# Optimization experiments

Hardware: AMD Instinct MI355X
Metric: run time of the kernel (lower is better)

## Reference

```python
import jax, jax.numpy as jnp
import numpy as np

N, E, D, H = 50000, 1600000, 256, 256
EPS = 1e-5

def prelu(x, a):
    return jnp.where(x >= 0, x, a * x)

def batch_norm(x, gamma, beta):
    # training-mode BatchNorm1d: stats over the node (batch) dim
    mu = jnp.mean(x, axis=0)
    var = jnp.var(x, axis=0)
    return (x - mu) * jax.lax.rsqrt(var + EPS) * gamma + beta

def gcn_conv(x, edge_index, W, b):
    # PyG GCNConv: h = XW, add self-loops, symmetric norm, scatter-add, + bias
    h = x @ W
    n = x.shape[0]
    row = jnp.concatenate([edge_index[0], jnp.arange(n)])
    col = jnp.concatenate([edge_index[1], jnp.arange(n)])
    w = jnp.ones(row.shape[0], dtype=x.dtype)
    deg = jax.ops.segment_sum(w, col, num_segments=n)
    dinv = jnp.where(deg > 0, jax.lax.rsqrt(deg), 0.0)
    norm = dinv[row] * w * dinv[col]  # [E+N]
    msg = h[row] * norm[:, None]      # [E+N, H] gathered messages
    out = jax.ops.segment_sum(msg, col, num_segments=n)
    return out + b

def setup_inputs() -> dict:
    key = jax.random.key(0)
    ks = jax.random.split(key, 10)
    x = jax.random.normal(ks[0], (N, D), dtype=jnp.float32)
    edge_index = jax.random.randint(ks[1], (2, E), 0, N).astype(jnp.int64)
    s1 = 1.0 / np.sqrt(D)
    s2 = 1.0 / np.sqrt(H)
    return {
        "x": x,
        "edge_index": edge_index,
        "W1": jax.random.uniform(ks[2], (D, H), jnp.float32, -s1, s1),
        "b1": jnp.zeros((H,), jnp.float32),
        "W2": jax.random.uniform(ks[3], (H, H), jnp.float32, -s2, s2),
        "b2": jnp.zeros((H,), jnp.float32),
        "prelu_a": jnp.asarray(0.25, jnp.float32),
        "bn_gamma": jnp.ones((H,), jnp.float32),
        "bn_beta": jnp.zeros((H,), jnp.float32),
        "proj_W": jax.random.uniform(ks[4], (H, H), jnp.float32, -s2, s2),
        "proj_b": jnp.zeros((H,), jnp.float32),
        "pbn_gamma": jnp.ones((H,), jnp.float32),
        "pbn_beta": jnp.zeros((H,), jnp.float32),
        "prelu2_a": jnp.asarray(0.25, jnp.float32),
    }

def reference(x, edge_index, W1, b1, W2, b2, prelu_a, bn_gamma, bn_beta,
              proj_W, proj_b, pbn_gamma, pbn_beta, prelu2_a):
    # eval-mode dropout (identity); BN uses batch stats
    z = prelu(gcn_conv(x, edge_index, W1, b1), prelu_a)
    z = prelu(gcn_conv(z, edge_index, W2, b2), prelu_a)
    z = batch_norm(z, bn_gamma, bn_beta)
    p = prelu(batch_norm(z @ proj_W + proj_b, pbn_gamma, pbn_beta), prelu2_a)
    return (z, p)
```

## Files before the change

kernel.cpp:

```cpp
#include <hip/hip_runtime.h>
#include <hip/hip_bf16.h>


#define CAP 96
#define NPB 128
#define CHUNK 4096
#define SEGBIG 4608
#define MAXBKT 512

typedef __attribute__((ext_vector_type(8))) short short8;
typedef __attribute__((ext_vector_type(4))) float f32x4;

__device__ __forceinline__ float bf2f(unsigned short u) {
    union { unsigned int i; float f; } v; v.i = ((unsigned int)u) << 16; return v.f;
}
__device__ __forceinline__ unsigned short f2bf(float f) {
    __hip_bfloat16 h = __float2bfloat16(f);
    return *reinterpret_cast<unsigned short*>(&h);
}

__global__ __launch_bounds__(256) void k_zero(int* segcnt, int nbkt, float* stats, float* dinv, int N) {
    int i = blockIdx.x * 256 + threadIdx.x;
    if (i < nbkt) segcnt[i] = 0;
    if (i < 2048) stats[i] = 0.0f;
    if (i == 0) dinv[N] = 0.0f;
}

__global__ __launch_bounds__(256) void k_zrow(unsigned short* hs, int N) {
    ((ushort4*)hs)[(size_t)N * 64 + threadIdx.x % 64] = ushort4{0, 0, 0, 0};
}

__global__ __launch_bounds__(256) void k_binh(const int* __restrict__ row, const int* __restrict__ col,
                                              unsigned* __restrict__ bins, int* __restrict__ segcnt,
                                              int E, int nbkt) {
    __shared__ int hist[MAXBKT];
    __shared__ int base[MAXBKT];
    int e0 = blockIdx.x * CHUNK;
    int eend = e0 + CHUNK; if (eend > E) eend = E;
    for (int b = threadIdx.x; b < nbkt; b += 256) hist[b] = 0;
    __syncthreads();
    for (int e = e0 + threadIdx.x; e < eend; e += 256)
        atomicAdd(&hist[col[e] >> 7], 1);
    __syncthreads();
    for (int b = threadIdx.x; b < nbkt; b += 256) {
        int h = hist[b];
        base[b] = h ? atomicAdd(&segcnt[b], h) : 0;
        hist[b] = 0;
    }
    __syncthreads();
    for (int e = e0 + threadIdx.x; e < eend; e += 256) {
        int v = col[e], r = row[e];
        int b = v >> 7;
        int p = base[b] + atomicAdd(&hist[b], 1);
        if (p < SEGBIG) bins[(size_t)b * SEGBIG + p] = ((unsigned)r << 7) | (unsigned)(v & (NPB - 1));
    }
}

__global__ __launch_bounds__(256) void k_csr(const unsigned* __restrict__ bins, const int* __restrict__ segcnt,
                                             int* __restrict__ csr, int* __restrict__ fillp,
                                             float* __restrict__ dinv, int N) {
    __shared__ int cnt[NPB];
    int bkt = blockIdx.x;
    if (threadIdx.x < NPB) cnt[threadIdx.x] = 0;
    __syncthreads();
    int m = segcnt[bkt]; if (m > SEGBIG) m = SEGBIG;
    const unsigned* b = bins + (size_t)bkt * SEGBIG;
    for (int i = threadIdx.x; i < m; i += 256) {
        unsigned ent = b[i];
        int loc = (int)(ent & (NPB - 1));
        int r   = (int)(ent >> 7);
        int p = atomicAdd(&cnt[loc], 1);
        if (p < CAP) csr[(size_t)(bkt * NPB + loc) * CAP + p] = r;
    }
    __syncthreads();
    if (threadIdx.x < NPB) {
        int v = bkt * NPB + threadIdx.x;
        if (v < N) {
            int c = cnt[threadIdx.x];
            int real = c < CAP ? c : CAP;
            int pc = (real + 15) & ~15;
            if (pc > CAP) pc = CAP;
            int* lst = csr + (size_t)v * CAP;
            for (int p = real; p < pc; ++p) lst[p] = N;
            fillp[v] = pc;
            dinv[v] = rsqrtf(1.0f + (float)c);
        }
    }
}

__global__ __launch_bounds__(256) void k_castx(const float* __restrict__ x, unsigned short* __restrict__ xb, size_t n4) {
    size_t stride = (size_t)gridDim.x * blockDim.x;
    for (size_t i = (size_t)blockIdx.x * blockDim.x + threadIdx.x; i < n4; i += stride) {
        float4 v = ((const float4*)x)[i];
        ushort4 o; o.x = f2bf(v.x); o.y = f2bf(v.y); o.z = f2bf(v.z); o.w = f2bf(v.w);
        ((ushort4*)xb)[i] = o;
    }
}

__global__ __launch_bounds__(256) void k_wt(const float* __restrict__ W, unsigned short* __restrict__ Wt) {
    __shared__ float t[32][33];
    int bx = blockIdx.x * 32, by = blockIdx.y * 32;
    int x = threadIdx.x & 31, y = threadIdx.x >> 5;
#pragma unroll
    for (int i = 0; i < 32; i += 8)
        t[y + i][x] = W[(size_t)(by + y + i) * 256 + bx + x];
    __syncthreads();
#pragma unroll
    for (int i = 0; i < 32; i += 8)
        Wt[(size_t)(bx + y + i) * 256 + by + x] = f2bf(t[x][y + i]);
}

__global__ __launch_bounds__(256) void k_gemm_bf16(const unsigned short* __restrict__ A,
                                                   const unsigned short* __restrict__ Bt,
                                                   unsigned short* __restrict__ C,
                                                   const float* __restrict__ dinv,
                                                   int use_scale, int M) {
    __shared__ unsigned short buf[16384];
    unsigned short* As = buf;
    unsigned short* Bs = buf + 8192;
    int tid  = threadIdx.x;
    int lane = tid & 63, wid = tid >> 6;
    int wr = wid >> 1, wc = wid & 1;
    int row0 = blockIdx.x * 128;
    int col0 = blockIdx.y * 128;

    f32x4 acc[4][4];
#pragma unroll
    for (int m = 0; m < 4; ++m)
#pragma unroll
        for (int n = 0; n < 4; ++n) acc[m][n] = f32x4{0.f, 0.f, 0.f, 0.f};

    int srow = lane >> 3;
    int sk   = (lane & 7) * 8;

    for (int k0 = 0; k0 < 256; k0 += 64) {
#pragma unroll
        for (int i = 0; i < 4; ++i) {
            int u = i * 4 + wid;
            int arow = row0 + u * 8 + srow;
            if (arow >= M) arow = M - 1;
            const unsigned short* ga = A  + (size_t)arow * 256 + k0 + sk;
            const unsigned short* gb = Bt + (size_t)(col0 + u * 8 + srow) * 256 + k0 + sk;
            __builtin_amdgcn_global_load_lds((const __attribute__((address_space(1))) void*)ga,
                (__attribute__((address_space(3))) void*)(As + u * 512), 16, 0, 0);
            __builtin_amdgcn_global_load_lds((const __attribute__((address_space(1))) void*)gb,
                (__attribute__((address_space(3))) void*)(Bs + u * 512), 16, 0, 0);
        }
        __syncthreads();
#pragma unroll
        for (int kk = 0; kk < 64; kk += 32) {
            short8 a[4], b[4];
#pragma unroll
            for (int m = 0; m < 4; ++m)
                a[m] = *(const short8*)(As + (wr * 64 + m * 16 + (lane & 15)) * 64 + kk + (lane >> 4) * 8);
#pragma unroll
            for (int n = 0; n < 4; ++n)
                b[n] = *(const short8*)(Bs + (wc * 64 + n * 16 + (lane & 15)) * 64 + kk + (lane >> 4) * 8);
#pragma unroll
            for (int m = 0; m < 4; ++m)
#pragma unroll
                for (int n = 0; n < 4; ++n)
                    acc[m][n] = __builtin_amdgcn_mfma_f32_16x16x32_bf16(a[m], b[n], acc[m][n], 0, 0, 0);
        }
        __syncthreads();
    }

#pragma unroll
    for (int m = 0; m < 4; ++m)
#pragma unroll
        for (int r = 0; r < 4; ++r) {
            int lr = wr * 64 + m * 16 + (lane >> 4) * 4 + r;
#pragma unroll
            for (int n = 0; n < 4; ++n)
                buf[lr * 128 + wc * 64 + n * 16 + (lane & 15)] = f2bf(acc[m][n][r]);
        }
    __syncthreads();
#pragma unroll
    for (int j = 0; j < 8; ++j) {
        int c = j * 256 + tid;
        int r = c >> 4, cc = c & 15;
        int grow = row0 + r;
        if (grow < M) {
            short8 v = *(const short8*)(buf + r * 128 + cc * 8);
            if (use_scale) {
                float d = dinv[grow];
                short8 o;
#pragma unroll
                for (int t = 0; t < 8; ++t)
                    o[t] = (short)f2bf(bf2f((unsigned short)v[t]) * d);
                v = o;
            }
            *(short8*)(C + (size_t)grow * 256 + col0 + cc * 8) = v;
        }
    }
}

__global__ __launch_bounds__(256) void k_agg_bf(const unsigned short* __restrict__ hs,
                                                unsigned short* __restrict__ outb,
                                                const float* __restrict__ dinv, const int* __restrict__ csr,
                                                const int* __restrict__ fillp, const float* __restrict__ bias,
                                                const float* __restrict__ aptr, int N) {
    int wv = threadIdx.x >> 6, lane = threadIdx.x & 63;
    int v = blockIdx.x * 4 + wv;
    if (v >= N) return;
    const ushort4* h4 = (const ushort4*)hs;
    float dv = dinv[v];
    ushort4 hv = h4[(size_t)v * 64 + lane];
    float s0 = bf2f(hv.x), s1 = bf2f(hv.y), s2 = bf2f(hv.z), s3 = bf2f(hv.w);
    int n = fillp[v];
    const int* lst = csr + (size_t)v * CAP;
    for (int i = 0; i < n; i += 16) {
        int u[16];
        ushort4 a[16];
#pragma unroll
        for (int t = 0; t < 16; ++t) u[t] = lst[i + t];
#pragma unroll
        for (int t = 0; t < 16; ++t) a[t] = h4[(size_t)u[t] * 64 + lane];
#pragma unroll
        for (int t = 0; t < 16; ++t) {
            s0 += bf2f(a[t].x); s1 += bf2f(a[t].y);
            s2 += bf2f(a[t].z); s3 += bf2f(a[t].w);
        }
    }
    float al = *aptr;
    float4 bb = *(const float4*)(bias + lane * 4);
    float o0 = dv * s0 + bb.x, o1 = dv * s1 + bb.y, o2 = dv * s2 + bb.z, o3 = dv * s3 + bb.w;
    o0 = o0 >= 0.f ? o0 : al * o0;
    o1 = o1 >= 0.f ? o1 : al * o1;
    o2 = o2 >= 0.f ? o2 : al * o2;
    o3 = o3 >= 0.f ? o3 : al * o3;
    ushort4 o; o.x = f2bf(o0); o.y = f2bf(o1); o.z = f2bf(o2); o.w = f2bf(o3);
    ((ushort4*)outb)[(size_t)v * 64 + lane] = o;
}

__global__ __launch_bounds__(256) void k_bnstats_v(const unsigned short* __restrict__ X, float* __restrict__ sums, int N) {
    int w = threadIdx.x >> 6, lane = threadIdx.x & 63;
    int c4 = lane * 4;
    float4 s = {0.f, 0.f, 0.f, 0.f}, q = {0.f, 0.f, 0.f, 0.f};
    int rstride = gridDim.x * 4;
    for (int r = blockIdx.x * 4 + w; r < N; r += rstride) {
        ushort4 x4 = ((const ushort4*)X)[(size_t)r * 64 + lane];
        float a = bf2f(x4.x), b = bf2f(x4.y), c = bf2f(x4.z), d = bf2f(x4.w);
        s.x += a; s.y += b; s.z += c; s.w += d;
        q.x += a * a; q.y += b * b; q.z += c * c; q.w += d * d;
    }
    atomicAdd(&sums[c4 + 0], s.x); atomicAdd(&sums[c4 + 1], s.y);
    atomicAdd(&sums[c4 + 2], s.z); atomicAdd(&sums[c4 + 3], s.w);
    atomicAdd(&sums[256 + c4 + 0], q.x); atomicAdd(&sums[256 + c4 + 1], q.y);
    atomicAdd(&sums[256 + c4 + 2], q.z); atomicAdd(&sums[256 + c4 + 3], q.w);
}

__global__ __launch_bounds__(256) void k_bnfinal(float* stats, const float* __restrict__ gamma,
                                                 const float* __restrict__ beta, float invN) {
    int c = threadIdx.x;
    float mu = stats[c] * invN;
    float var = stats[256 + c] * invN - mu * mu;
    float rstd = rsqrtf(var + 1e-5f);
    float sc = rstd * gamma[c];
    stats[512 + c] = sc;
    stats[768 + c] = beta[c] - mu * sc;
}

__global__ __launch_bounds__(256) void k_bnapply_z(const unsigned short* __restrict__ in,
                                                   float* __restrict__ zout, unsigned short* __restrict__ zb,
                                                   const float* __restrict__ scale, const float* __restrict__ shift,
                                                   size_t n4) {
    size_t stride = (size_t)gridDim.x * blockDim.x;
    for (size_t i = (size_t)blockIdx.x * blockDim.x + threadIdx.x; i < n4; i += stride) {
        int c4 = (int)(i & 63) * 4;
        ushort4 x4 = ((const ushort4*)in)[i];
        float4 sc = *(const float4*)(scale + c4);
        float4 sh = *(const float4*)(shift + c4);
        float4 y;
        y.x = bf2f(x4.x) * sc.x + sh.x;
        y.y = bf2f(x4.y) * sc.y + sh.y;
        y.z = bf2f(x4.z) * sc.z + sh.z;
        y.w = bf2f(x4.w) * sc.w + sh.w;
        ((float4*)zout)[i] = y;
        ushort4 o; o.x = f2bf(y.x); o.y = f2bf(y.y); o.z = f2bf(y.z); o.w = f2bf(y.w);
        ((ushort4*)zb)[i] = o;
    }
}

__global__ __launch_bounds__(256) void k_bnapply_p(const unsigned short* __restrict__ in,
                                                   float* __restrict__ pout,
                                                   const float* __restrict__ scale, const float* __restrict__ shift,
                                                   const float* __restrict__ aptr, size_t n4) {
    size_t stride = (size_t)gridDim.x * blockDim.x;
    float a = *aptr;
    for (size_t i = (size_t)blockIdx.x * blockDim.x + threadIdx.x; i < n4; i += stride) {
        int c4 = (int)(i & 63) * 4;
        ushort4 x4 = ((const ushort4*)in)[i];
        float4 sc = *(const float4*)(scale + c4);
        float4 sh = *(const float4*)(shift + c4);
        float4 y;
        y.x = bf2f(x4.x) * sc.x + sh.x;
        y.y = bf2f(x4.y) * sc.y + sh.y;
        y.z = bf2f(x4.z) * sc.z + sh.z;
        y.w = bf2f(x4.w) * sc.w + sh.w;
        y.x = y.x >= 0.f ? y.x : a * y.x;
        y.y = y.y >= 0.f ? y.y : a * y.y;
        y.z = y.z >= 0.f ? y.z : a * y.z;
        y.w = y.w >= 0.f ? y.w : a * y.w;
        ((float4*)pout)[i] = y;
    }
}

extern "C" void kernel_launch(void* const* d_in, const int* in_sizes, int n_in,
                              void* d_out, int out_size, void* d_ws, size_t ws_size,
                              hipStream_t stream) {
    const float* x     = (const float*)d_in[0];
    const int*   ei    = (const int*)d_in[1];
    const float* W1    = (const float*)d_in[2];
    const float* b1    = (const float*)d_in[3];
    const float* W2    = (const float*)d_in[4];
    const float* b2    = (const float*)d_in[5];
    const float* aptr  = (const float*)d_in[6];
    const float* gamma = (const float*)d_in[7];
    const float* beta  = (const float*)d_in[8];
    const float* projW = (const float*)d_in[9];
    const float* pgamma = (const float*)d_in[11];
    const float* pbeta  = (const float*)d_in[12];
    const float* a2ptr  = (const float*)d_in[13];

    int N = in_sizes[0] / 256;
    int E = in_sizes[1] / 2;
    const int* row = ei;
    const int* col = ei + E;

    float* out  = (float*)d_out;
    float* zout = out;
    float* pout = out + (size_t)N * 256;

    int nbkt = (N + NPB - 1) / NPB;

    size_t rowsz = (size_t)(N + 1) * 256;
    unsigned short* B0 = (unsigned short*)d_ws;
    unsigned short* B1 = B0 + rowsz;
    unsigned short* B2 = B1 + rowsz;
    unsigned short* Wt = B2 + rowsz;
    float* dinv  = (float*)(Wt + 3 * 65536);
    int*   fillp = (int*)(dinv + N + 1);
    int*   csr   = fillp + N;
    float* stats = (float*)(csr + (size_t)N * CAP);
    int*   segcnt= (int*)(stats + 2048);
    unsigned* bins = (unsigned*)(segcnt + MAXBKT);

    int nb_binh = (E + CHUNK - 1) / CHUNK;
    dim3 ggrid((N + 127) / 128, 2);
    dim3 wgrid(8, 8);
    int  agrid = (N + 3) / 4;
    size_t n4 = (size_t)N * 64;

    k_zero <<<8, 256, 0, stream>>>(segcnt, nbkt, stats, dinv, N);
    k_zrow <<<1, 64, 0, stream>>>(B1, N);
    k_binh <<<nb_binh, 256, 0, stream>>>(row, col, bins, segcnt, E, nbkt);
    k_csr  <<<nbkt, 256, 0, stream>>>(bins, segcnt, csr, fillp, dinv, N);
    k_castx<<<2048, 256, 0, stream>>>(x, B0, n4);
    k_wt   <<<wgrid, 256, 0, stream>>>(W1,    Wt);
    k_wt   <<<wgrid, 256, 0, stream>>>(W2,    Wt + 65536);
    k_wt   <<<wgrid, 256, 0, stream>>>(projW, Wt + 131072);

    k_gemm_bf16<<<ggrid, 256, 0, stream>>>(B0, Wt, B1, dinv, 1, N);
    k_agg_bf   <<<agrid, 256, 0, stream>>>(B1, B2, dinv, csr, fillp, b1, aptr, N);
    k_zrow <<<1, 64, 0, stream>>>(B1, N);
    k_gemm_bf16<<<ggrid, 256, 0, stream>>>(B2, Wt + 65536, B1, dinv, 1, N);
    k_agg_bf   <<<agrid, 256, 0, stream>>>(B1, B0, dinv, csr, fillp, b2, aptr, N);
    k_bnstats_v<<<128, 256, 0, stream>>>(B0, stats, N);
    k_bnfinal  <<<1, 256, 0, stream>>>(stats, gamma, beta, 1.0f / (float)N);
    k_bnapply_z<<<2048, 256, 0, stream>>>(B0, zout, B2, stats + 512, stats + 768, n4);
    k_gemm_bf16<<<ggrid, 256, 0, stream>>>(B2, Wt + 131072, B1, dinv, 0, N);
    k_bnstats_v<<<128, 256, 0, stream>>>(B1, stats + 1024, N);
    k_bnfinal  <<<1, 256, 0, stream>>>(stats + 1024, pgamma, pbeta, 1.0f / (float)N);
    k_bnapply_p<<<2048, 256, 0, stream>>>(B1, pout, stats + 1536, stats + 1792, a2ptr, n4);
}
```

Baseline: 677.3 us.

## Fold first BatchNorm into projection weights and refine edge binning granularity

The BN scale is folded into the transposed projection weights, and the shift becomes a per-column bias vector computed by a small kernel and added in the GEMM epilogue. This lets the projection GEMM read the pre-BN aggregate directly, and removes the bf16 write of the normalized z. Edge binning now uses 64-node buckets with smaller chunks, and the per-bucket counters are padded to separate cache lines to reduce atomic contention. It also drops one zero-row launch and the dinv[N] initialization. The trade-offs are an extra serial 256-thread matvec kernel, and bf16 rounding now applied to the pre-BN values times folded weights, which changes numerics slightly.

```diff
diff --git a/kernel.cpp b/kernel.cpp
--- a/kernel.cpp
+++ b/kernel.cpp
@@ -3,10 +3,11 @@
 
 
 #define CAP 96
-#define NPB 128
-#define CHUNK 4096
-#define SEGBIG 4608
-#define MAXBKT 512
+#define NPB 64
+#define CHUNK 2048
+#define SEGBIG 2432
+#define MAXBKT 1024
+#define SEGSTR 16
 
 typedef __attribute__((ext_vector_type(8))) short short8;
 typedef __attribute__((ext_vector_type(4))) float f32x4;
@@ -19,15 +20,14 @@
     return *reinterpret_cast<unsigned short*>(&h);
 }
 
-__global__ __launch_bounds__(256) void k_zero(int* segcnt, int nbkt, float* stats, float* dinv, int N) {
+__global__ __launch_bounds__(256) void k_zero(int* segcnt, int nbkt, float* stats) {
     int i = blockIdx.x * 256 + threadIdx.x;
-    if (i < nbkt) segcnt[i] = 0;
+    if (i < nbkt * SEGSTR) segcnt[i] = 0;
     if (i < 2048) stats[i] = 0.0f;
-    if (i == 0) dinv[N] = 0.0f;
-}
-
-__global__ __launch_bounds__(256) void k_zrow(unsigned short* hs, int N) {
-    ((ushort4*)hs)[(size_t)N * 64 + threadIdx.x % 64] = ushort4{0, 0, 0, 0};
+}
+
+__global__ __launch_bounds__(64) void k_zrow(unsigned short* hs, int N) {
+    ((ushort4*)hs)[(size_t)N * 64 + threadIdx.x] = ushort4{0, 0, 0, 0};
 }
 
 __global__ __launch_bounds__(256) void k_binh(const int* __restrict__ row, const int* __restrict__ col,
@@ -40,19 +40,19 @@
     for (int b = threadIdx.x; b < nbkt; b += 256) hist[b] = 0;
     __syncthreads();
     for (int e = e0 + threadIdx.x; e < eend; e += 256)
-        atomicAdd(&hist[col[e] >> 7], 1);
+        atomicAdd(&hist[col[e] >> 6], 1);
     __syncthreads();
     for (int b = threadIdx.x; b < nbkt; b += 256) {
         int h = hist[b];
-        base[b] = h ? atomicAdd(&segcnt[b], h) : 0;
+        base[b] = h ? atomicAdd(&segcnt[b * SEGSTR], h) : 0;
         hist[b] = 0;
     }
     __syncthreads();
     for (int e = e0 + threadIdx.x; e < eend; e += 256) {
         int v = col[e], r = row[e];
-        int b = v >> 7;
+        int b = v >> 6;
         int p = base[b] + atomicAdd(&hist[b], 1);
-        if (p < SEGBIG) bins[(size_t)b * SEGBIG + p] = ((unsigned)r << 7) | (unsigned)(v & (NPB - 1));
+        if (p < SEGBIG) bins[(size_t)b * SEGBIG + p] = ((unsigned)r << 6) | (unsigned)(v & (NPB - 1));
     }
 }
 
@@ -63,12 +63,12 @@
     int bkt = blockIdx.x;
     if (threadIdx.x < NPB) cnt[threadIdx.x] = 0;
     __syncthreads();
-    int m = segcnt[bkt]; if (m > SEGBIG) m = SEGBIG;
+    int m = segcnt[bkt * SEGSTR]; if (m > SEGBIG) m = SEGBIG;
     const unsigned* b = bins + (size_t)bkt * SEGBIG;
     for (int i = threadIdx.x; i < m; i += 256) {
         unsigned ent = b[i];
         int loc = (int)(ent & (NPB - 1));
-        int r   = (int)(ent >> 7);
+        int r   = (int)(ent >> 6);
         int p = atomicAdd(&cnt[loc], 1);
         if (p < CAP) csr[(size_t)(bkt * NPB + loc) * CAP + p] = r;
     }
@@ -97,24 +97,36 @@
     }
 }
 
-__global__ __launch_bounds__(256) void k_wt(const float* __restrict__ W, unsigned short* __restrict__ Wt) {
+__global__ __launch_bounds__(256) void k_wt(const float* __restrict__ W, unsigned short* __restrict__ Wt,
+                                            const float* __restrict__ scp) {
     __shared__ float t[32][33];
     int bx = blockIdx.x * 32, by = blockIdx.y * 32;
     int x = threadIdx.x & 31, y = threadIdx.x >> 5;
 #pragma unroll
-    for (int i = 0; i < 32; i += 8)
-        t[y + i][x] = W[(size_t)(by + y + i) * 256 + bx + x];
+    for (int i = 0; i < 32; i += 8) {
+        float s = scp ? scp[by + y + i] : 1.0f;
+        t[y + i][x] = W[(size_t)(by + y + i) * 256 + bx + x] * s;
+    }
     __syncthreads();
 #pragma unroll
     for (int i = 0; i < 32; i += 8)
         Wt[(size_t)(bx + y + i) * 256 + by + x] = f2bf(t[x][y + i]);
+}
+
+__global__ __launch_bounds__(256) void k_tvec(const float* __restrict__ W, const float* __restrict__ sh,
+                                              float* __restrict__ tvec) {
+    int n = threadIdx.x;
+    float s = 0.0f;
+    for (int k = 0; k < 256; ++k) s += sh[k] * W[(size_t)k * 256 + n];
+    tvec[n] = s;
 }
 
 __global__ __launch_bounds__(256) void k_gemm_bf16(const unsigned short* __restrict__ A,
                                                    const unsigned short* __restrict__ Bt,
                                                    unsigned short* __restrict__ C,
-                                                   const float* __restrict__ dinv,
-                                                   int use_scale, int M) {
+                                                   const float* __restrict__ dinv, int use_scale,
+                                                   const float* __restrict__ tvec, int use_bias,
+                                                   int M) {
     __shared__ unsigned short buf[16384];
     unsigned short* As = buf;
     unsigned short* Bs = buf + 8192;
@@ -165,6 +177,11 @@
         __syncthreads();
     }
 
+    float tn[4] = {0.f, 0.f, 0.f, 0.f};
+    if (use_bias) {
+#pragma unroll
+        for (int n = 0; n < 4; ++n) tn[n] = tvec[col0 + wc * 64 + n * 16 + (lane & 15)];
+    }
 #pragma unroll
     for (int m = 0; m < 4; ++m)
 #pragma unroll
@@ -172,7 +189,7 @@
             int lr = wr * 64 + m * 16 + (lane >> 4) * 4 + r;
 #pragma unroll
             for (int n = 0; n < 4; ++n)
-                buf[lr * 128 + wc * 64 + n * 16 + (lane & 15)] = f2bf(acc[m][n][r]);
+                buf[lr * 128 + wc * 64 + n * 16 + (lane & 15)] = f2bf(acc[m][n][r] + tn[n]);
         }
     __syncthreads();
 #pragma unroll
@@ -262,7 +279,7 @@
 }
 
 __global__ __launch_bounds__(256) void k_bnapply_z(const unsigned short* __restrict__ in,
-                                                   float* __restrict__ zout, unsigned short* __restrict__ zb,
+                                                   float* __restrict__ zout,
                                                    const float* __restrict__ scale, const float* __restrict__ shift,
                                                    size_t n4) {
     size_t stride = (size_t)gridDim.x * blockDim.x;
@@ -277,8 +294,6 @@
         y.z = bf2f(x4.z) * sc.z + sh.z;
         y.w = bf2f(x4.w) * sc.w + sh.w;
         ((float4*)zout)[i] = y;
-        ushort4 o; o.x = f2bf(y.x); o.y = f2bf(y.y); o.z = f2bf(y.z); o.w = f2bf(y.w);
-        ((ushort4*)zb)[i] = o;
     }
 }
 
@@ -343,8 +358,9 @@
     int*   fillp = (int*)(dinv + N + 1);
     int*   csr   = fillp + N;
     float* stats = (float*)(csr + (size_t)N * CAP);
-    int*   segcnt= (int*)(stats + 2048);
-    unsigned* bins = (unsigned*)(segcnt + MAXBKT);
+    float* tvec  = stats + 2048;
+    int*   segcnt= (int*)(tvec + 256);
+    unsigned* bins = (unsigned*)(segcnt + (size_t)nbkt * SEGSTR);
 
     int nb_binh = (E + CHUNK - 1) / CHUNK;
     dim3 ggrid((N + 127) / 128, 2);
@@ -352,24 +368,24 @@
     int  agrid = (N + 3) / 4;
     size_t n4 = (size_t)N * 64;
 
-    k_zero <<<8, 256, 0, stream>>>(segcnt, nbkt, stats, dinv, N);
+    k_zero <<<64, 256, 0, stream>>>(segcnt, nbkt, stats);
     k_zrow <<<1, 64, 0, stream>>>(B1, N);
     k_binh <<<nb_binh, 256, 0, stream>>>(row, col, bins, segcnt, E, nbkt);
     k_csr  <<<nbkt, 256, 0, stream>>>(bins, segcnt, csr, fillp, dinv, N);
     k_castx<<<2048, 256, 0, stream>>>(x, B0, n4);
-    k_wt   <<<wgrid, 256, 0, stream>>>(W1,    Wt);
-    k_wt   <<<wgrid, 256, 0, stream>>>(W2,    Wt + 65536);
-    k_wt   <<<wgrid, 256, 0, stream>>>(projW, Wt + 131072);
-
-    k_gemm_bf16<<<ggrid, 256, 0, stream>>>(B0, Wt, B1, dinv, 1, N);
+    k_wt   <<<wgrid, 256, 0, stream>>>(W1, Wt,         nullptr);
+    k_wt   <<<wgrid, 256, 0, stream>>>(W2, Wt + 65536, nullptr);
+
+    k_gemm_bf16<<<ggrid, 256, 0, stream>>>(B0, Wt, B1, dinv, 1, nullptr, 0, N);
     k_agg_bf   <<<agrid, 256, 0, stream>>>(B1, B2, dinv, csr, fillp, b1, aptr, N);
-    k_zrow <<<1, 64, 0, stream>>>(B1, N);
-    k_gemm_bf16<<<ggrid, 256, 0, stream>>>(B2, Wt + 65536, B1, dinv, 1, N);
+    k_gemm_bf16<<<ggrid, 256, 0, stream>>>(B2, Wt + 65536, B1, dinv, 1, nullptr, 0, N);
     k_agg_bf   <<<agrid, 256, 0, stream>>>(B1, B0, dinv, csr, fillp, b2, aptr, N);
     k_bnstats_v<<<128, 256, 0, stream>>>(B0, stats, N);
     k_bnfinal  <<<1, 256, 0, stream>>>(stats, gamma, beta, 1.0f / (float)N);
-    k_bnapply_z<<<2048, 256, 0, stream>>>(B0, zout, B2, stats + 512, stats + 768, n4);
-    k_gemm_bf16<<<ggrid, 256, 0, stream>>>(B2, Wt + 131072, B1, dinv, 0, N);
+    k_wt   <<<wgrid, 256, 0, stream>>>(projW, Wt + 131072, stats + 512);
+    k_tvec <<<1, 256, 0, stream>>>(projW, stats + 768, tvec);
+    k_gemm_bf16<<<ggrid, 256, 0, stream>>>(B0, Wt + 131072, B1, dinv, 0, tvec, 1, N);
+    k_bnapply_z<<<2048, 256, 0, stream>>>(B0, zout, stats + 512, stats + 768, n4);
     k_bnstats_v<<<128, 256, 0, stream>>>(B1, stats + 1024, N);
     k_bnfinal  <<<1, 256, 0, stream>>>(stats + 1024, pgamma, pbeta, 1.0f / (float)N);
     k_bnapply_p<<<2048, 256, 0, stream>>>(B1, pout, stats + 1536, stats + 1792, a2ptr, n4);
```

Result: slower. 721.8 us (+6.6%).
